# Performance work log

Hardware: AMD Instinct MI355X
Metric: run time of the kernel (lower is better)

The kernel has to match this reference:

```python
import jax, jax.numpy as jnp
import numpy as np

B, N, D = 16, 1024, 128


def setup_inputs() -> dict:
    key = jax.random.key(0)
    ks = jax.random.split(key, 12)
    x = jax.random.normal(ks[0], (B, N, D), dtype=jnp.float32)
    # binary symmetric-ish adjacency mask (0/1 floats)
    adj = jax.random.randint(ks[1], (B, N, N), 0, 2).astype(jnp.float32)
    Ww = jax.random.normal(ks[2], (D, D), dtype=jnp.float32) * 0.05
    Wb = jax.random.normal(ks[3], (D,), dtype=jnp.float32) * 0.05
    A = jax.random.normal(ks[4], (D, D), dtype=jnp.float32) * 0.05
    wi_u = jax.random.normal(ks[5], (D,), dtype=jnp.float32) * 0.05
    wi_x = jax.random.normal(ks[6], (D,), dtype=jnp.float32) * 0.05
    wf_u = jax.random.normal(ks[7], (D,), dtype=jnp.float32) * 0.05
    wf_x = jax.random.normal(ks[8], (D,), dtype=jnp.float32) * 0.05
    wo_u = jax.random.normal(ks[9], (D,), dtype=jnp.float32) * 0.05
    wo_x = jax.random.normal(ks[10], (D,), dtype=jnp.float32) * 0.05
    return {"x": x, "adj": adj, "Ww": Ww, "Wb": Wb, "A": A,
            "wi_u": wi_u, "wi_x": wi_x, "wf_u": wf_u, "wf_x": wf_x,
            "wo_u": wo_u, "wo_x": wo_x}


def reference(x, adj, Ww, Wb, A, wi_u, wi_x, wf_u, wf_x, wo_u, wo_x):
    # h = W(x): [B,N,D]
    h = jnp.einsum('bnf,df->bnd', x, Ww) + Wb
    # e[b,j,k] = (h A) . h  -> symmetrized dense scores [B,N,N]
    e = jnp.einsum('bjl,bkl->bjk', jnp.einsum('bjd,dl->bjl', h, A), h)
    e = e + jnp.swapaxes(e, 1, 2)
    # masked softmax over axis=1 (columns), then re-mask by adj
    scores = jnp.where(adj > 0, e, 0.0)
    attention = jax.nn.softmax(scores, axis=1) * adj
    # aggregation
    h_prime = jax.nn.relu(jnp.einsum('bij,bjk->bik', attention, h))
    # LSTM-style gates: scalar per node, broadcast over features
    ic = jax.nn.sigmoid(h_prime @ wi_u + x @ wi_x)[..., None]
    fc = jax.nn.sigmoid(h_prime @ wf_u + x @ wf_x)[..., None]
    oc = jax.nn.sigmoid(h_prime @ wo_u + x @ wo_x)[..., None]
    return oc * jnp.tanh(ic * h_prime + fc * x)
```

## Files before the change

### kernel.cpp

```cpp
#include <hip/hip_runtime.h>


#define B_ 16
#define N_ 1024
#define D_ 128

typedef __attribute__((ext_vector_type(8))) short bf16x8;
typedef __attribute__((ext_vector_type(4))) float f32x4;

__device__ __forceinline__ float b2f(unsigned short u) {
    union { unsigned int i; float f; } v; v.i = ((unsigned int)u) << 16; return v.f;
}
__device__ __forceinline__ unsigned short f2b(float f) {
    union { float f; unsigned int i; } v; v.f = f;
    unsigned int x = v.i;
    return (unsigned short)((x + 0x7fffu + ((x >> 16) & 1u)) >> 16);
}
__device__ __forceinline__ float clamp60(float v) {
    return fminf(fmaxf(v, -60.f), 60.f);
}
__device__ __forceinline__ bf16x8 load8f(const float* p) {
    float4 a = *reinterpret_cast<const float4*>(p);
    float4 b = *reinterpret_cast<const float4*>(p + 4);
    bf16x8 v;
    v[0] = (short)f2b(a.x); v[1] = (short)f2b(a.y);
    v[2] = (short)f2b(a.z); v[3] = (short)f2b(a.w);
    v[4] = (short)f2b(b.x); v[5] = (short)f2b(b.y);
    v[6] = (short)f2b(b.z); v[7] = (short)f2b(b.w);
    return v;
}

__global__ __launch_bounds__(256) void k0_w2t(
    const float* __restrict__ Ww, const float* __restrict__ Wb,
    const float* __restrict__ A, unsigned short* __restrict__ WwB,
    unsigned short* __restrict__ W2T, float* __restrict__ wbA) {
    int t = blockIdx.x * 256 + threadIdx.x;
    int l = t >> 7, f = t & 127;
    float acc = 0.f;
    for (int d = 0; d < 128; ++d)
        acc += A[d * 128 + l] * Ww[d * 128 + f];
    W2T[l * 128 + f] = f2b(acc);
    WwB[t] = f2b(Ww[t]);
    if (blockIdx.x == 0 && threadIdx.x < 128) {
        float s = 0.f;
        for (int d = 0; d < 128; ++d) s += Wb[d] * A[d * 128 + threadIdx.x];
        wbA[threadIdx.x] = s;
    }
}

__global__ __launch_bounds__(256) void kmask(
    const float* __restrict__ adj, unsigned long long* __restrict__ maskJ) {
    int w = threadIdx.x >> 6, lane = threadIdx.x & 63;
    size_t base = ((size_t)blockIdx.x * 4 + w) * 256;
    unsigned long long w0 = __ballot(adj[base + 0 * 64 + lane] > 0.f);
    unsigned long long w1 = __ballot(adj[base + 1 * 64 + lane] > 0.f);
    unsigned long long w2 = __ballot(adj[base + 2 * 64 + lane] > 0.f);
    unsigned long long w3 = __ballot(adj[base + 3 * 64 + lane] > 0.f);
    unsigned long long o = lane == 0 ? w0 : lane == 1 ? w1 : lane == 2 ? w2 : w3;
    if (lane < 4) maskJ[(base >> 6) + lane] = o;
}

__global__ __launch_bounds__(256) void k1_hu(
    const float* __restrict__ x, const unsigned short* __restrict__ WwB,
    const float* __restrict__ Wb, const unsigned short* __restrict__ W2T,
    const float* __restrict__ wbA,
    unsigned short* __restrict__ h, unsigned short* __restrict__ u,
    unsigned short* __restrict__ hT) {
    __shared__ unsigned short lds[16][128];
    int w = threadIdx.x >> 6, lane = threadIdx.x & 63;
    int c = lane & 15, q = lane >> 4;
    int rowbase = blockIdx.x * 16;
    int b = rowbase >> 10;
    int n0 = rowbase & 1023;

    bf16x8 xa[4];
    const float* xrow = x + (size_t)(rowbase + c) * 128;
#pragma unroll
    for (int ks = 0; ks < 4; ++ks)
        xa[ks] = load8f(xrow + ks * 32 + q * 8);

#pragma unroll
    for (int tt = 0; tt < 2; ++tt) {
        int t = w * 2 + tt;
        f32x4 acch = {0.f, 0.f, 0.f, 0.f};
        f32x4 accu = {0.f, 0.f, 0.f, 0.f};
        const unsigned short* wwrow = WwB + (t * 16 + c) * 128;
        const unsigned short* w2row = W2T + (t * 16 + c) * 128;
#pragma unroll
        for (int ks = 0; ks < 4; ++ks) {
            bf16x8 bw = *reinterpret_cast<const bf16x8*>(wwrow + ks * 32 + q * 8);
            bf16x8 b2 = *reinterpret_cast<const bf16x8*>(w2row + ks * 32 + q * 8);
            acch = __builtin_amdgcn_mfma_f32_16x16x32_bf16(xa[ks], bw, acch, 0, 0, 0);
            accu = __builtin_amdgcn_mfma_f32_16x16x32_bf16(xa[ks], b2, accu, 0, 0, 0);
        }
        float wb = Wb[t * 16 + c];
        float ub = wbA[t * 16 + c];
#pragma unroll
        for (int r = 0; r < 4; ++r) {
            int row = rowbase + q * 4 + r;
            unsigned short hv = f2b(acch[r] + wb);
            unsigned short uv = f2b(accu[r] + ub);
            h[(size_t)row * 128 + t * 16 + c] = hv;
            u[(size_t)row * 128 + t * 16 + c] = uv;
            lds[q * 4 + r][t * 16 + c] = hv;
        }
    }
    __syncthreads();
    int tid = threadIdx.x;
    if (tid < 128) {
        int d = tid;
        unsigned int p[8];
#pragma unroll
        for (int k = 0; k < 8; ++k) {
            unsigned int v0 = lds[2 * k][d], v1 = lds[2 * k + 1][d];
            p[k] = v0 | (v1 << 16);
        }
        size_t basehT = ((size_t)(b * 128 + d)) * 1024 + n0;
        uint4* dst = reinterpret_cast<uint4*>(hT + basehT);
        dst[0] = make_uint4(p[0], p[1], p[2], p[3]);
        dst[1] = make_uint4(p[4], p[5], p[6], p[7]);
    }
}


__global__ __launch_bounds__(256) void k2_scores(
    const unsigned short* __restrict__ h, const unsigned short* __restrict__ u,
    const unsigned long long* __restrict__ maskJ,
    unsigned short* __restrict__ att, float* __restrict__ colpart) {
    __shared__ unsigned long long lmask[16][16];
    int w = threadIdx.x >> 6, lane = threadIdx.x & 63;
    int c = lane & 15, q = lane >> 4;
    int b = blockIdx.x >> 6;
    int iblk = blockIdx.x & 63;
    int i0 = iblk * 16;
    const unsigned short* hb = h + (size_t)b * N_ * D_;
    const unsigned short* ub = u + (size_t)b * N_ * D_;

    lmask[threadIdx.x >> 4][threadIdx.x & 15] =
        maskJ[(size_t)(b * 1024 + i0 + (threadIdx.x >> 4)) * 16 + (threadIdx.x & 15)];
    __syncthreads();

    bf16x8 Au[4], Ah[4];
#pragma unroll
    for (int ks = 0; ks < 4; ++ks) {
        Au[ks] = *reinterpret_cast<const bf16x8*>(ub + (i0 + c) * 128 + ks * 32 + q * 8);
        Ah[ks] = *reinterpret_cast<const bf16x8*>(hb + (i0 + c) * 128 + ks * 32 + q * 8);
    }
    unsigned short* attrow = att + ((size_t)(b * 1024 + i0)) * 1024;
    float* cprow = colpart + ((size_t)(b * 64 + iblk)) * 1024;

    int jt0 = w * 16;
    bf16x8 Bh[2][4], Bu[2][4];
#pragma unroll
    for (int s = 0; s < 2; ++s) {
        int jg = (jt0 + s) * 16;
#pragma unroll
        for (int ks = 0; ks < 4; ++ks) {
            Bh[s][ks] = *reinterpret_cast<const bf16x8*>(hb + (jg + c) * 128 + ks * 32 + q * 8);
            Bu[s][ks] = *reinterpret_cast<const bf16x8*>(ub + (jg + c) * 128 + ks * 32 + q * 8);
        }
    }
#pragma unroll
    for (int t = 0; t < 16; ++t) {
        int jt = jt0 + t, j0 = jt * 16;
        int slot = t & 1;
        f32x4 a1 = {0.f, 0.f, 0.f, 0.f};
        f32x4 a2 = {0.f, 0.f, 0.f, 0.f};
#pragma unroll
        for (int ks = 0; ks < 4; ++ks) {
            a1 = __builtin_amdgcn_mfma_f32_16x16x32_bf16(Au[ks], Bh[slot][ks], a1, 0, 0, 0);
            a2 = __builtin_amdgcn_mfma_f32_16x16x32_bf16(Ah[ks], Bu[slot][ks], a2, 0, 0, 0);
        }
        if (t < 14) {
            int jn = (jt + 2) * 16;
#pragma unroll
            for (int ks = 0; ks < 4; ++ks) {
                Bh[slot][ks] = *reinterpret_cast<const bf16x8*>(hb + (jn + c) * 128 + ks * 32 + q * 8);
                Bu[slot][ks] = *reinterpret_cast<const bf16x8*>(ub + (jn + c) * 128 + ks * 32 + q * 8);
            }
        }
        int wd = jt >> 2, sh = (jt & 3) * 16;
        float colp = 0.f;
#pragma unroll
        for (int r = 0; r < 4; ++r) {
            float e = a1[r] + a2[r];
            bool m = (lmask[q * 4 + r][wd] >> (sh + c)) & 1ull;
            float ex = m ? __expf(clamp60(e)) : 0.f;
            colp += m ? ex : 1.0f;
            attrow[(size_t)(q * 4 + r) * 1024 + j0 + c] = f2b(ex);
        }
        colp += __shfl_xor(colp, 16, 64);
        colp += __shfl_xor(colp, 32, 64);
        if (q == 0) cprow[j0 + c] = colp;
    }
}

__global__ __launch_bounds__(256) void k2b_recip(
    const float* __restrict__ colpart, float* __restrict__ rl0) {
    int g = blockIdx.x * 256 + threadIdx.x;
    int b = g >> 10, j = g & 1023;
    float s = 0.f;
    const float* p = colpart + (size_t)b * 64 * 1024 + j;
    for (int ib = 0; ib < 64; ++ib) s += p[(size_t)ib * 1024];
    rl0[g] = 1.0f / s;
}

__global__ __launch_bounds__(256) void k3_gemm(
    const unsigned short* __restrict__ att, const float* __restrict__ rl0,
    const unsigned short* __restrict__ hT, const float* __restrict__ x,
    const float* __restrict__ wi_u, const float* __restrict__ wi_x,
    const float* __restrict__ wf_u, const float* __restrict__ wf_x,
    const float* __restrict__ wo_u, const float* __restrict__ wo_x,
    float* __restrict__ out) {
    __shared__ float red[4][16][129];
    int w = threadIdx.x >> 6, lane = threadIdx.x & 63;
    int c = lane & 15, q = lane >> 4;
    int b = blockIdx.x >> 6;
    int i0 = (blockIdx.x & 63) * 16;
    const unsigned short* attrow = att + ((size_t)(b * 1024 + i0 + c)) * 1024;
    const unsigned short* hTb = hT + (size_t)b * 128 * 1024;
    const float* rl0b = rl0 + b * 1024;

    f32x4 hp[8];
#pragma unroll
    for (int t = 0; t < 8; ++t) hp[t] = (f32x4){0.f, 0.f, 0.f, 0.f};

#pragma unroll
    for (int tt = 0; tt < 8; ++tt) {
        int jp = w * 8 + tt;
        int jb = jp * 32 + q * 8;
        bf16x8 eraw = *reinterpret_cast<const bf16x8*>(attrow + jb);
        float4 r0 = *reinterpret_cast<const float4*>(rl0b + jb);
        float4 r1 = *reinterpret_cast<const float4*>(rl0b + jb + 4);
        bf16x8 a;
        a[0] = (short)f2b(b2f((unsigned short)eraw[0]) * r0.x);
        a[1] = (short)f2b(b2f((unsigned short)eraw[1]) * r0.y);
        a[2] = (short)f2b(b2f((unsigned short)eraw[2]) * r0.z);
        a[3] = (short)f2b(b2f((unsigned short)eraw[3]) * r0.w);
        a[4] = (short)f2b(b2f((unsigned short)eraw[4]) * r1.x);
        a[5] = (short)f2b(b2f((unsigned short)eraw[5]) * r1.y);
        a[6] = (short)f2b(b2f((unsigned short)eraw[6]) * r1.z);
        a[7] = (short)f2b(b2f((unsigned short)eraw[7]) * r1.w);
#pragma unroll
        for (int t = 0; t < 8; ++t) {
            bf16x8 bt = *reinterpret_cast<const bf16x8*>(
                hTb + (size_t)(t * 16 + c) * 1024 + jp * 32 + q * 8);
            hp[t] = __builtin_amdgcn_mfma_f32_16x16x32_bf16(a, bt, hp[t], 0, 0, 0);
        }
    }

#pragma unroll
    for (int t = 0; t < 8; ++t)
#pragma unroll
        for (int r = 0; r < 4; ++r)
            red[w][q * 4 + r][t * 16 + c] = hp[t][r];
    __syncthreads();
    if (w != 0) return;

#pragma unroll
    for (int t = 0; t < 8; ++t)
#pragma unroll
        for (int r = 0; r < 4; ++r)
            hp[t][r] = red[0][q * 4 + r][t * 16 + c] + red[1][q * 4 + r][t * 16 + c]
                     + red[2][q * 4 + r][t * 16 + c] + red[3][q * 4 + r][t * 16 + c];

    float xv[8][4];
#pragma unroll
    for (int t = 0; t < 8; ++t)
#pragma unroll
        for (int r = 0; r < 4; ++r) {
            hp[t][r] = fmaxf(hp[t][r], 0.f);
            xv[t][r] = x[(size_t)(b * 1024 + i0 + q * 4 + r) * 128 + t * 16 + c];
        }
    float wiu[8], wix[8], wfu[8], wfx[8], wou[8], wox[8];
#pragma unroll
    for (int t = 0; t < 8; ++t) {
        wiu[t] = wi_u[t * 16 + c]; wix[t] = wi_x[t * 16 + c];
        wfu[t] = wf_u[t * 16 + c]; wfx[t] = wf_x[t * 16 + c];
        wou[t] = wo_u[t * 16 + c]; wox[t] = wo_x[t * 16 + c];
    }
#pragma unroll
    for (int r = 0; r < 4; ++r) {
        float zi = 0.f, zf = 0.f, zo = 0.f;
#pragma unroll
        for (int t = 0; t < 8; ++t) {
            zi += hp[t][r] * wiu[t] + xv[t][r] * wix[t];
            zf += hp[t][r] * wfu[t] + xv[t][r] * wfx[t];
            zo += hp[t][r] * wou[t] + xv[t][r] * wox[t];
        }
        zi += __shfl_xor(zi, 1, 64); zi += __shfl_xor(zi, 2, 64);
        zi += __shfl_xor(zi, 4, 64); zi += __shfl_xor(zi, 8, 64);
        zf += __shfl_xor(zf, 1, 64); zf += __shfl_xor(zf, 2, 64);
        zf += __shfl_xor(zf, 4, 64); zf += __shfl_xor(zf, 8, 64);
        zo += __shfl_xor(zo, 1, 64); zo += __shfl_xor(zo, 2, 64);
        zo += __shfl_xor(zo, 4, 64); zo += __shfl_xor(zo, 8, 64);
        float ic = 1.f / (1.f + __expf(-zi));
        float fc = 1.f / (1.f + __expf(-zf));
        float oc = 1.f / (1.f + __expf(-zo));
#pragma unroll
        for (int t = 0; t < 8; ++t) {
            float zz = ic * hp[t][r] + fc * xv[t][r];
            float th = 1.f - 2.f / (__expf(2.f * zz) + 1.f);
            out[(size_t)(b * 1024 + i0 + q * 4 + r) * 128 + t * 16 + c] = oc * th;
        }
    }
}

__global__ __launch_bounds__(256) void k2_stats(
    const unsigned short* __restrict__ h, const unsigned short* __restrict__ u,
    const unsigned long long* __restrict__ maskJ, float* __restrict__ rl0) {
    int w = threadIdx.x >> 6, lane = threadIdx.x & 63;
    int c = lane & 15, q = lane >> 4;
    int b = blockIdx.x >> 6;
    int j0 = (blockIdx.x & 63) * 16;
    const unsigned short* hb = h + (size_t)b * N_ * D_;
    const unsigned short* ub = u + (size_t)b * N_ * D_;

    bf16x8 Bh[4], Bu[4];
#pragma unroll
    for (int ks = 0; ks < 4; ++ks) {
        Bh[ks] = *reinterpret_cast<const bf16x8*>(hb + (j0 + c) * 128 + ks * 32 + q * 8);
        Bu[ks] = *reinterpret_cast<const bf16x8*>(ub + (j0 + c) * 128 + ks * 32 + q * 8);
    }
    float colsum = 0.f;
    const unsigned long long* mrow = maskJ + (size_t)b * 1024 * 16 + (j0 >> 6);
    int jb = j0 & 63;

    for (int it = w; it < 64; it += 4) {
        int i0 = it * 16;
        f32x4 acc = {0.f, 0.f, 0.f, 0.f};
#pragma unroll
        for (int ks = 0; ks < 4; ++ks) {
            bf16x8 au = *reinterpret_cast<const bf16x8*>(ub + (i0 + c) * 128 + ks * 32 + q * 8);
            bf16x8 ah = *reinterpret_cast<const bf16x8*>(hb + (i0 + c) * 128 + ks * 32 + q * 8);
            acc = __builtin_amdgcn_mfma_f32_16x16x32_bf16(au, Bh[ks], acc, 0, 0, 0);
            acc = __builtin_amdgcn_mfma_f32_16x16x32_bf16(ah, Bu[ks], acc, 0, 0, 0);
        }
#pragma unroll
        for (int r = 0; r < 4; ++r) {
            int i = i0 + q * 4 + r;
            unsigned long long mword = mrow[(size_t)i * 16];
            bool m = (mword >> (jb + c)) & 1ull;
            colsum += m ? __expf(clamp60(acc[r])) : 1.0f;
        }
    }
    colsum += __shfl_xor(colsum, 16, 64);
    colsum += __shfl_xor(colsum, 32, 64);
    __shared__ float part[4][16];
    if (lane < 16) part[w][lane] = colsum;
    __syncthreads();
    if (threadIdx.x < 16) {
        float s = part[0][threadIdx.x] + part[1][threadIdx.x]
                + part[2][threadIdx.x] + part[3][threadIdx.x];
        rl0[b * 1024 + j0 + threadIdx.x] = 1.0f / s;
    }
}

__global__ __launch_bounds__(256) void k3_fused(
    const unsigned short* __restrict__ h, const unsigned short* __restrict__ uu,
    const unsigned long long* __restrict__ maskJ, const float* __restrict__ rl0,
    const unsigned short* __restrict__ hT, const float* __restrict__ x,
    const float* __restrict__ wi_u, const float* __restrict__ wi_x,
    const float* __restrict__ wf_u, const float* __restrict__ wf_x,
    const float* __restrict__ wo_u, const float* __restrict__ wo_x,
    float* __restrict__ out) {
    __shared__ float red[4][16][129];
    int w = threadIdx.x >> 6, lane = threadIdx.x & 63;
    int c = lane & 15, q = lane >> 4;
    int b = blockIdx.x >> 6;
    int i0 = (blockIdx.x & 63) * 16;
    const unsigned short* hb = h + (size_t)b * N_ * D_;
    const unsigned short* ub = uu + (size_t)b * N_ * D_;
    const unsigned short* hTb = hT + (size_t)b * 128 * 1024;
    const unsigned long long* mrowI = maskJ + (size_t)(b * 1024 + i0 + c) * 16;
    const float* rl0b = rl0 + b * 1024;

    bf16x8 Bh[4], Bu[4];
#pragma unroll
    for (int ks = 0; ks < 4; ++ks) {
        Bh[ks] = *reinterpret_cast<const bf16x8*>(hb + (i0 + c) * 128 + ks * 32 + q * 8);
        Bu[ks] = *reinterpret_cast<const bf16x8*>(ub + (i0 + c) * 128 + ks * 32 + q * 8);
    }
    f32x4 hp[8];
#pragma unroll
    for (int t = 0; t < 8; ++t) hp[t] = (f32x4){0.f, 0.f, 0.f, 0.f};

    for (int jp = w; jp < 32; jp += 4) {
        int j0 = jp * 32;
        unsigned long long mw64 = mrowI[jp >> 1];
        unsigned int mbits = (unsigned int)(mw64 >> ((jp & 1) * 32));
        unsigned int u00, u01, u10, u11;
#pragma unroll
        for (int s = 0; s < 2; ++s) {
            int js = j0 + s * 16;
            f32x4 acc = {0.f, 0.f, 0.f, 0.f};
#pragma unroll
            for (int ks = 0; ks < 4; ++ks) {
                bf16x8 au = *reinterpret_cast<const bf16x8*>(ub + (js + c) * 128 + ks * 32 + q * 8);
                bf16x8 ah = *reinterpret_cast<const bf16x8*>(hb + (js + c) * 128 + ks * 32 + q * 8);
                acc = __builtin_amdgcn_mfma_f32_16x16x32_bf16(au, Bh[ks], acc, 0, 0, 0);
                acc = __builtin_amdgcn_mfma_f32_16x16x32_bf16(ah, Bu[ks], acc, 0, 0, 0);
            }
            float4 rv = *reinterpret_cast<const float4*>(rl0b + js + q * 4);
            int bb = s * 16 + q * 4;
            float a0 = ((mbits >> (bb + 0)) & 1u) ? __expf(clamp60(acc[0])) * rv.x : 0.f;
            float a1 = ((mbits >> (bb + 1)) & 1u) ? __expf(clamp60(acc[1])) * rv.y : 0.f;
            float a2 = ((mbits >> (bb + 2)) & 1u) ? __expf(clamp60(acc[2])) * rv.z : 0.f;
            float a3 = ((mbits >> (bb + 3)) & 1u) ? __expf(clamp60(acc[3])) * rv.w : 0.f;
            unsigned int p0 = (unsigned int)f2b(a0) | ((unsigned int)f2b(a1) << 16);
            unsigned int p1 = (unsigned int)f2b(a2) | ((unsigned int)f2b(a3) << 16);
            if (s == 0) { u00 = p0; u01 = p1; } else { u10 = p0; u11 = p1; }
        }
        int la = c + 32 * (q & 1);
        int lb = la + 16;
        unsigned int x0 = __shfl((int)u00, la, 64), x1 = __shfl((int)u01, la, 64);
        unsigned int x2 = __shfl((int)u00, lb, 64), x3 = __shfl((int)u01, lb, 64);
        unsigned int y0 = __shfl((int)u10, la, 64), y1 = __shfl((int)u11, la, 64);
        unsigned int y2 = __shfl((int)u10, lb, 64), y3 = __shfl((int)u11, lb, 64);
        bool hiq = (q >> 1) != 0;
        union { unsigned int ui[4]; bf16x8 v; } att;
        att.ui[0] = hiq ? y0 : x0;
        att.ui[1] = hiq ? y1 : x1;
        att.ui[2] = hiq ? y2 : x2;
        att.ui[3] = hiq ? y3 : x3;
#pragma unroll
        for (int t = 0; t < 8; ++t) {
            bf16x8 bt = *reinterpret_cast<const bf16x8*>(
                hTb + (size_t)(t * 16 + c) * 1024 + j0 + q * 8);
            hp[t] = __builtin_amdgcn_mfma_f32_16x16x32_bf16(att.v, bt, hp[t], 0, 0, 0);
        }
    }

#pragma unroll
    for (int t = 0; t < 8; ++t)
#pragma unroll
        for (int r = 0; r < 4; ++r)
            red[w][q * 4 + r][t * 16 + c] = hp[t][r];
    __syncthreads();
    if (w != 0) return;

#pragma unroll
    for (int t = 0; t < 8; ++t)
#pragma unroll
        for (int r = 0; r < 4; ++r)
            hp[t][r] = red[0][q * 4 + r][t * 16 + c] + red[1][q * 4 + r][t * 16 + c]
                     + red[2][q * 4 + r][t * 16 + c] + red[3][q * 4 + r][t * 16 + c];

    float xv[8][4];
#pragma unroll
    for (int t = 0; t < 8; ++t)
#pragma unroll
        for (int r = 0; r < 4; ++r) {
            hp[t][r] = fmaxf(hp[t][r], 0.f);
            xv[t][r] = x[(size_t)(b * 1024 + i0 + q * 4 + r) * 128 + t * 16 + c];
        }
    float wiu[8], wix[8], wfu[8], wfx[8], wou[8], wox[8];
#pragma unroll
    for (int t = 0; t < 8; ++t) {
        wiu[t] = wi_u[t * 16 + c]; wix[t] = wi_x[t * 16 + c];
        wfu[t] = wf_u[t * 16 + c]; wfx[t] = wf_x[t * 16 + c];
        wou[t] = wo_u[t * 16 + c]; wox[t] = wo_x[t * 16 + c];
    }
#pragma unroll
    for (int r = 0; r < 4; ++r) {
        float zi = 0.f, zf = 0.f, zo = 0.f;
#pragma unroll
        for (int t = 0; t < 8; ++t) {
            zi += hp[t][r] * wiu[t] + xv[t][r] * wix[t];
            zf += hp[t][r] * wfu[t] + xv[t][r] * wfx[t];
            zo += hp[t][r] * wou[t] + xv[t][r] * wox[t];
        }
        zi += __shfl_xor(zi, 1, 64); zi += __shfl_xor(zi, 2, 64);
        zi += __shfl_xor(zi, 4, 64); zi += __shfl_xor(zi, 8, 64);
        zf += __shfl_xor(zf, 1, 64); zf += __shfl_xor(zf, 2, 64);
        zf += __shfl_xor(zf, 4, 64); zf += __shfl_xor(zf, 8, 64);
        zo += __shfl_xor(zo, 1, 64); zo += __shfl_xor(zo, 2, 64);
        zo += __shfl_xor(zo, 4, 64); zo += __shfl_xor(zo, 8, 64);
        float ic = 1.f / (1.f + __expf(-zi));
        float fc = 1.f / (1.f + __expf(-zf));
        float oc = 1.f / (1.f + __expf(-zo));
#pragma unroll
        for (int t = 0; t < 8; ++t) {
            float zz = ic * hp[t][r] + fc * xv[t][r];
            float th = 1.f - 2.f / (__expf(2.f * zz) + 1.f);
            out[(size_t)(b * 1024 + i0 + q * 4 + r) * 128 + t * 16 + c] = oc * th;
        }
    }
}

extern "C" void kernel_launch(void* const* d_in, const int* in_sizes, int n_in,
                              void* d_out, int out_size, void* d_ws, size_t ws_size,
                              hipStream_t stream) {
    const float* x    = (const float*)d_in[0];
    const float* adj  = (const float*)d_in[1];
    const float* Ww   = (const float*)d_in[2];
    const float* Wb   = (const float*)d_in[3];
    const float* A    = (const float*)d_in[4];
    const float* wi_u = (const float*)d_in[5];
    const float* wi_x = (const float*)d_in[6];
    const float* wf_u = (const float*)d_in[7];
    const float* wf_x = (const float*)d_in[8];
    const float* wo_u = (const float*)d_in[9];
    const float* wo_x = (const float*)d_in[10];
    float* out = (float*)d_out;
    char* ws = (char*)d_ws;

    if (ws_size >= (56ull << 20)) {
        unsigned short* WwB = (unsigned short*)(ws);
        unsigned short* W2T = (unsigned short*)(ws + (32u << 10));
        float* wbA          = (float*)(ws + (64u << 10));
        float* rl0          = (float*)(ws + (128u << 10));
        unsigned long long* maskJ = (unsigned long long*)(ws + (256u << 10));
        float* colpart      = (float*)(ws + (4ull << 20));
        unsigned short* h   = (unsigned short*)(ws + (8ull << 20));
        unsigned short* u   = (unsigned short*)(ws + (12ull << 20));
        unsigned short* hT  = (unsigned short*)(ws + (16ull << 20));
        unsigned short* att = (unsigned short*)(ws + (20ull << 20));

        k0_w2t<<<64, 256, 0, stream>>>(Ww, Wb, A, WwB, W2T, wbA);
        kmask<<<16384, 256, 0, stream>>>(adj, maskJ);
        k1_hu<<<1024, 256, 0, stream>>>(x, WwB, Wb, W2T, wbA, h, u, hT);
        k2_scores<<<1024, 256, 0, stream>>>(h, u, maskJ, att, colpart);
        k2b_recip<<<64, 256, 0, stream>>>(colpart, rl0);
        k3_gemm<<<1024, 256, 0, stream>>>(att, rl0, hT, x,
                                          wi_u, wi_x, wf_u, wf_x, wo_u, wo_x, out);
    } else {
        unsigned short* WwB = (unsigned short*)(ws);
        unsigned short* W2T = (unsigned short*)(ws + (32u << 10));
        float* wbA          = (float*)(ws + (64u << 10));
        float* rl0          = (float*)(ws + (128u << 10));
        unsigned short* h   = (unsigned short*)(ws + (1u << 20));
        unsigned short* u   = (unsigned short*)(ws + (5u << 20));
        unsigned short* hT  = (unsigned short*)(ws + (9u << 20));
        unsigned long long* maskJ = (unsigned long long*)(ws + (13u << 20));

        k0_w2t<<<64, 256, 0, stream>>>(Ww, Wb, A, WwB, W2T, wbA);
        kmask<<<16384, 256, 0, stream>>>(adj, maskJ);
        k1_hu<<<1024, 256, 0, stream>>>(x, WwB, Wb, W2T, wbA, h, u, hT);
        k2_stats<<<1024, 256, 0, stream>>>(h, u, maskJ, rl0);
        k3_fused<<<1024, 256, 0, stream>>>(h, u, maskJ, rl0, hT, x,
                                           wi_u, wi_x, wf_u, wf_x, wo_u, wo_x, out);
    }
}
```

Measured before the change: 249.9 us.

## Fuse adjacency bitmask build into k1 and tile scores over 32 rows

```diff
diff --git a/kernel.cpp b/kernel.cpp
--- a/kernel.cpp
+++ b/kernel.cpp
@@ -63,9 +63,9 @@
 __global__ __launch_bounds__(256) void k1_hu(
     const float* __restrict__ x, const unsigned short* __restrict__ WwB,
     const float* __restrict__ Wb, const unsigned short* __restrict__ W2T,
-    const float* __restrict__ wbA,
+    const float* __restrict__ wbA, const float* __restrict__ adj,
     unsigned short* __restrict__ h, unsigned short* __restrict__ u,
-    unsigned short* __restrict__ hT) {
+    unsigned short* __restrict__ hT, unsigned long long* __restrict__ maskJ) {
     __shared__ unsigned short lds[16][128];
     int w = threadIdx.x >> 6, lane = threadIdx.x & 63;
     int c = lane & 15, q = lane >> 4;
@@ -105,6 +105,19 @@
             lds[q * 4 + r][t * 16 + c] = hv;
         }
     }
+
+    {
+        const float* adjb = adj + ((size_t)(rowbase + w * 4)) * 1024;
+#pragma unroll
+        for (int r = 0; r < 4; ++r) {
+#pragma unroll
+            for (int g = 0; g < 16; ++g) {
+                unsigned long long m = __ballot(adjb[(size_t)r * 1024 + g * 64 + lane] > 0.f);
+                if (lane == 0) maskJ[(size_t)(rowbase + w * 4 + r) * 16 + g] = m;
+            }
+        }
+    }
+
     __syncthreads();
     int tid = threadIdx.x;
     if (tid < 128) {
@@ -127,67 +140,69 @@
     const unsigned short* __restrict__ h, const unsigned short* __restrict__ u,
     const unsigned long long* __restrict__ maskJ,
     unsigned short* __restrict__ att, float* __restrict__ colpart) {
-    __shared__ unsigned long long lmask[16][16];
+    __shared__ unsigned long long lmask[32][16];
     int w = threadIdx.x >> 6, lane = threadIdx.x & 63;
     int c = lane & 15, q = lane >> 4;
-    int b = blockIdx.x >> 6;
-    int iblk = blockIdx.x & 63;
-    int i0 = iblk * 16;
+    int b = blockIdx.x >> 5;
+    int iblk = blockIdx.x & 31;
+    int i0 = iblk * 32;
     const unsigned short* hb = h + (size_t)b * N_ * D_;
     const unsigned short* ub = u + (size_t)b * N_ * D_;
 
-    lmask[threadIdx.x >> 4][threadIdx.x & 15] =
-        maskJ[(size_t)(b * 1024 + i0 + (threadIdx.x >> 4)) * 16 + (threadIdx.x & 15)];
+    {
+        int tid = threadIdx.x;
+        lmask[tid >> 4][tid & 15] =
+            maskJ[(size_t)(b * 1024 + i0 + (tid >> 4)) * 16 + (tid & 15)];
+        lmask[16 + (tid >> 4)][tid & 15] =
+            maskJ[(size_t)(b * 1024 + i0 + 16 + (tid >> 4)) * 16 + (tid & 15)];
+    }
     __syncthreads();
 
-    bf16x8 Au[4], Ah[4];
+    bf16x8 Au0[4], Ah0[4], Au1[4], Ah1[4];
 #pragma unroll
     for (int ks = 0; ks < 4; ++ks) {
-        Au[ks] = *reinterpret_cast<const bf16x8*>(ub + (i0 + c) * 128 + ks * 32 + q * 8);
-        Ah[ks] = *reinterpret_cast<const bf16x8*>(hb + (i0 + c) * 128 + ks * 32 + q * 8);
+        Au0[ks] = *reinterpret_cast<const bf16x8*>(ub + (i0 + c) * 128 + ks * 32 + q * 8);
+        Ah0[ks] = *reinterpret_cast<const bf16x8*>(hb + (i0 + c) * 128 + ks * 32 + q * 8);
+        Au1[ks] = *reinterpret_cast<const bf16x8*>(ub + (i0 + 16 + c) * 128 + ks * 32 + q * 8);
+        Ah1[ks] = *reinterpret_cast<const bf16x8*>(hb + (i0 + 16 + c) * 128 + ks * 32 + q * 8);
     }
     unsigned short* attrow = att + ((size_t)(b * 1024 + i0)) * 1024;
-    float* cprow = colpart + ((size_t)(b * 64 + iblk)) * 1024;
+    float* cprow = colpart + ((size_t)(b * 32 + iblk)) * 1024;
 
     int jt0 = w * 16;
-    bf16x8 Bh[2][4], Bu[2][4];
-#pragma unroll
-    for (int s = 0; s < 2; ++s) {
-        int jg = (jt0 + s) * 16;
-#pragma unroll
-        for (int ks = 0; ks < 4; ++ks) {
-            Bh[s][ks] = *reinterpret_cast<const bf16x8*>(hb + (jg + c) * 128 + ks * 32 + q * 8);
-            Bu[s][ks] = *reinterpret_cast<const bf16x8*>(ub + (jg + c) * 128 + ks * 32 + q * 8);
-        }
-    }
 #pragma unroll
     for (int t = 0; t < 16; ++t) {
         int jt = jt0 + t, j0 = jt * 16;
-        int slot = t & 1;
-        f32x4 a1 = {0.f, 0.f, 0.f, 0.f};
-        f32x4 a2 = {0.f, 0.f, 0.f, 0.f};
+        bf16x8 Bh[4], Bu[4];
 #pragma unroll
         for (int ks = 0; ks < 4; ++ks) {
-            a1 = __builtin_amdgcn_mfma_f32_16x16x32_bf16(Au[ks], Bh[slot][ks], a1, 0, 0, 0);
-            a2 = __builtin_amdgcn_mfma_f32_16x16x32_bf16(Ah[ks], Bu[slot][ks], a2, 0, 0, 0);
-        }
-        if (t < 14) {
-            int jn = (jt + 2) * 16;
-#pragma unroll
-            for (int ks = 0; ks < 4; ++ks) {
-                Bh[slot][ks] = *reinterpret_cast<const bf16x8*>(hb + (jn + c) * 128 + ks * 32 + q * 8);
-                Bu[slot][ks] = *reinterpret_cast<const bf16x8*>(ub + (jn + c) * 128 + ks * 32 + q * 8);
-            }
+            Bh[ks] = *reinterpret_cast<const bf16x8*>(hb + (j0 + c) * 128 + ks * 32 + q * 8);
+            Bu[ks] = *reinterpret_cast<const bf16x8*>(ub + (j0 + c) * 128 + ks * 32 + q * 8);
+        }
+        f32x4 a00 = {0.f, 0.f, 0.f, 0.f};
+        f32x4 a01 = {0.f, 0.f, 0.f, 0.f};
+        f32x4 a10 = {0.f, 0.f, 0.f, 0.f};
+        f32x4 a11 = {0.f, 0.f, 0.f, 0.f};
+#pragma unroll
+        for (int ks = 0; ks < 4; ++ks) {
+            a00 = __builtin_amdgcn_mfma_f32_16x16x32_bf16(Au0[ks], Bh[ks], a00, 0, 0, 0);
+            a01 = __builtin_amdgcn_mfma_f32_16x16x32_bf16(Ah0[ks], Bu[ks], a01, 0, 0, 0);
+            a10 = __builtin_amdgcn_mfma_f32_16x16x32_bf16(Au1[ks], Bh[ks], a10, 0, 0, 0);
+            a11 = __builtin_amdgcn_mfma_f32_16x16x32_bf16(Ah1[ks], Bu[ks], a11, 0, 0, 0);
         }
         int wd = jt >> 2, sh = (jt & 3) * 16;
         float colp = 0.f;
 #pragma unroll
         for (int r = 0; r < 4; ++r) {
-            float e = a1[r] + a2[r];
-            bool m = (lmask[q * 4 + r][wd] >> (sh + c)) & 1ull;
-            float ex = m ? __expf(clamp60(e)) : 0.f;
-            colp += m ? ex : 1.0f;
-            attrow[(size_t)(q * 4 + r) * 1024 + j0 + c] = f2b(ex);
+            float e0 = a00[r] + a01[r];
+            float e1 = a10[r] + a11[r];
+            bool m0 = (lmask[q * 4 + r][wd] >> (sh + c)) & 1ull;
+            bool m1 = (lmask[16 + q * 4 + r][wd] >> (sh + c)) & 1ull;
+            float ex0 = m0 ? __expf(clamp60(e0)) : 0.f;
+            float ex1 = m1 ? __expf(clamp60(e1)) : 0.f;
+            colp += (m0 ? ex0 : 1.0f) + (m1 ? ex1 : 1.0f);
+            attrow[(size_t)(q * 4 + r) * 1024 + j0 + c] = f2b(ex0);
+            attrow[(size_t)(16 + q * 4 + r) * 1024 + j0 + c] = f2b(ex1);
         }
         colp += __shfl_xor(colp, 16, 64);
         colp += __shfl_xor(colp, 32, 64);
@@ -200,8 +215,8 @@
     int g = blockIdx.x * 256 + threadIdx.x;
     int b = g >> 10, j = g & 1023;
     float s = 0.f;
-    const float* p = colpart + (size_t)b * 64 * 1024 + j;
-    for (int ib = 0; ib < 64; ++ib) s += p[(size_t)ib * 1024];
+    const float* p = colpart + (size_t)b * 32 * 1024 + j;
+    for (int ib = 0; ib < 32; ++ib) s += p[(size_t)ib * 1024];
     rl0[g] = 1.0f / s;
 }
 
@@ -306,6 +321,66 @@
     }
 }
 
+__global__ __launch_bounds__(256) void k1_hu_nb(
+    const float* __restrict__ x, const unsigned short* __restrict__ WwB,
+    const float* __restrict__ Wb, const unsigned short* __restrict__ W2T,
+    const float* __restrict__ wbA,
+    unsigned short* __restrict__ h, unsigned short* __restrict__ u,
+    unsigned short* __restrict__ hT) {
+    __shared__ unsigned short lds[16][128];
+    int w = threadIdx.x >> 6, lane = threadIdx.x & 63;
+    int c = lane & 15, q = lane >> 4;
+    int rowbase = blockIdx.x * 16;
+    int b = rowbase >> 10;
+    int n0 = rowbase & 1023;
+    bf16x8 xa[4];
+    const float* xrow = x + (size_t)(rowbase + c) * 128;
+#pragma unroll
+    for (int ks = 0; ks < 4; ++ks)
+        xa[ks] = load8f(xrow + ks * 32 + q * 8);
+#pragma unroll
+    for (int tt = 0; tt < 2; ++tt) {
+        int t = w * 2 + tt;
+        f32x4 acch = {0.f, 0.f, 0.f, 0.f};
+        f32x4 accu = {0.f, 0.f, 0.f, 0.f};
+        const unsigned short* wwrow = WwB + (t * 16 + c) * 128;
+        const unsigned short* w2row = W2T + (t * 16 + c) * 128;
+#pragma unroll
+        for (int ks = 0; ks < 4; ++ks) {
+            bf16x8 bw = *reinterpret_cast<const bf16x8*>(wwrow + ks * 32 + q * 8);
+            bf16x8 b2 = *reinterpret_cast<const bf16x8*>(w2row + ks * 32 + q * 8);
+            acch = __builtin_amdgcn_mfma_f32_16x16x32_bf16(xa[ks], bw, acch, 0, 0, 0);
+            accu = __builtin_amdgcn_mfma_f32_16x16x32_bf16(xa[ks], b2, accu, 0, 0, 0);
+        }
+        float wb = Wb[t * 16 + c];
+        float ub = wbA[t * 16 + c];
+#pragma unroll
+        for (int r = 0; r < 4; ++r) {
+            int row = rowbase + q * 4 + r;
+            unsigned short hv = f2b(acch[r] + wb);
+            unsigned short uv = f2b(accu[r] + ub);
+            h[(size_t)row * 128 + t * 16 + c] = hv;
+            u[(size_t)row * 128 + t * 16 + c] = uv;
+            lds[q * 4 + r][t * 16 + c] = hv;
+        }
+    }
+    __syncthreads();
+    int tid = threadIdx.x;
+    if (tid < 128) {
+        int d = tid;
+        unsigned int p[8];
+#pragma unroll
+        for (int k = 0; k < 8; ++k) {
+            unsigned int v0 = lds[2 * k][d], v1 = lds[2 * k + 1][d];
+            p[k] = v0 | (v1 << 16);
+        }
+        size_t basehT = ((size_t)(b * 128 + d)) * 1024 + n0;
+        uint4* dst = reinterpret_cast<uint4*>(hT + basehT);
+        dst[0] = make_uint4(p[0], p[1], p[2], p[3]);
+        dst[1] = make_uint4(p[4], p[5], p[6], p[7]);
+    }
+}
+
 __global__ __launch_bounds__(256) void k2_stats(
     const unsigned short* __restrict__ h, const unsigned short* __restrict__ u,
     const unsigned long long* __restrict__ maskJ, float* __restrict__ rl0) {
@@ -315,7 +390,6 @@
     int j0 = (blockIdx.x & 63) * 16;
     const unsigned short* hb = h + (size_t)b * N_ * D_;
     const unsigned short* ub = u + (size_t)b * N_ * D_;
-
     bf16x8 Bh[4], Bu[4];
 #pragma unroll
     for (int ks = 0; ks < 4; ++ks) {
@@ -325,7 +399,6 @@
     float colsum = 0.f;
     const unsigned long long* mrow = maskJ + (size_t)b * 1024 * 16 + (j0 >> 6);
     int jb = j0 & 63;
-
     for (int it = w; it < 64; it += 4) {
         int i0 = it * 16;
         f32x4 acc = {0.f, 0.f, 0.f, 0.f};
@@ -374,7 +447,6 @@
     const unsigned short* hTb = hT + (size_t)b * 128 * 1024;
     const unsigned long long* mrowI = maskJ + (size_t)(b * 1024 + i0 + c) * 16;
     const float* rl0b = rl0 + b * 1024;
-
     bf16x8 Bh[4], Bu[4];
 #pragma unroll
     for (int ks = 0; ks < 4; ++ks) {
@@ -384,7 +456,6 @@
     f32x4 hp[8];
 #pragma unroll
     for (int t = 0; t < 8; ++t) hp[t] = (f32x4){0.f, 0.f, 0.f, 0.f};
-
     for (int jp = w; jp < 32; jp += 4) {
         int j0 = jp * 32;
         unsigned long long mw64 = mrowI[jp >> 1];
@@ -430,7 +501,6 @@
             hp[t] = __builtin_amdgcn_mfma_f32_16x16x32_bf16(att.v, bt, hp[t], 0, 0, 0);
         }
     }
-
 #pragma unroll
     for (int t = 0; t < 8; ++t)
 #pragma unroll
@@ -438,14 +508,12 @@
             red[w][q * 4 + r][t * 16 + c] = hp[t][r];
     __syncthreads();
     if (w != 0) return;
-
 #pragma unroll
     for (int t = 0; t < 8; ++t)
 #pragma unroll
         for (int r = 0; r < 4; ++r)
             hp[t][r] = red[0][q * 4 + r][t * 16 + c] + red[1][q * 4 + r][t * 16 + c]
                      + red[2][q * 4 + r][t * 16 + c] + red[3][q * 4 + r][t * 16 + c];
-
     float xv[8][4];
 #pragma unroll
     for (int t = 0; t < 8; ++t)
@@ -518,9 +586,8 @@
         unsigned short* att = (unsigned short*)(ws + (20ull << 20));
 
         k0_w2t<<<64, 256, 0, stream>>>(Ww, Wb, A, WwB, W2T, wbA);
-        kmask<<<16384, 256, 0, stream>>>(adj, maskJ);
-        k1_hu<<<1024, 256, 0, stream>>>(x, WwB, Wb, W2T, wbA, h, u, hT);
-        k2_scores<<<1024, 256, 0, stream>>>(h, u, maskJ, att, colpart);
+        k1_hu<<<1024, 256, 0, stream>>>(x, WwB, Wb, W2T, wbA, adj, h, u, hT, maskJ);
+        k2_scores<<<512, 256, 0, stream>>>(h, u, maskJ, att, colpart);
         k2b_recip<<<64, 256, 0, stream>>>(colpart, rl0);
         k3_gemm<<<1024, 256, 0, stream>>>(att, rl0, hT, x,
                                           wi_u, wi_x, wf_u, wf_x, wo_u, wo_x, out);
@@ -536,7 +603,7 @@
 
         k0_w2t<<<64, 256, 0, stream>>>(Ww, Wb, A, WwB, W2T, wbA);
         kmask<<<16384, 256, 0, stream>>>(adj, maskJ);
-        k1_hu<<<1024, 256, 0, stream>>>(x, WwB, Wb, W2T, wbA, h, u, hT);
+        k1_hu_nb<<<1024, 256, 0, stream>>>(x, WwB, Wb, W2T, wbA, h, u, hT);
         k2_stats<<<1024, 256, 0, stream>>>(h, u, maskJ, rl0);
         k3_fused<<<1024, 256, 0, stream>>>(h, u, maskJ, rl0, hT, x,
                                            wi_u, wi_x, wf_u, wf_x, wo_u, wo_x, out);
```

New measurement: 246.5 us. Within noise of the previous version (-1.3%).
